# Kernel optimization log

Measured on AMD Instinct MI355X. Metric: run time of the kernel, lower is better.

Reference implementation:

```python
import math
import jax, jax.numpy as jnp
import numpy as np


def setup_inputs() -> dict:
    key = jax.random.key(0)
    k1, k2, k3 = jax.random.split(key, 3)
    mk = jax.random.normal(k1, (4, 64, 8, 32, 32), dtype=jnp.float32)
    qk = jax.random.normal(k2, (4, 64, 32, 32), dtype=jnp.float32)
    mv = jax.random.normal(k3, (4, 512, 8, 32, 32), dtype=jnp.float32)
    return {"mk": mk, "qk": qk, "mv": mv}


def reference(mk, qk, mv):
    B, CK, T, H, W = mk.shape
    CV = mv.shape[1]
    mkf = mk.reshape(B, CK, T * H * W)          # [B, CK, N]  (memory tokens)
    qkf = qk.reshape(B, CK, H * W)              # [B, CK, M]  (query tokens)
    # L2-distance style affinity: (2*a.b - |a|^2) / sqrt(CK)
    a_sq = jnp.sum(mkf * mkf, axis=1)[:, :, None]              # [B, N, 1]
    ab = jnp.einsum('bcn,bcm->bnm', mkf, qkf)                  # [B, N, M]
    affinity = (2.0 * ab - a_sq) / math.sqrt(CK)
    affinity = jax.nn.softmax(affinity, axis=1)                # softmax over memory dim
    # readout: weighted sum of memory values
    mo = mv.reshape(B, CV, T * H * W)                          # [B, CV, N]
    mem = jnp.einsum('bcn,bnm->bcm', mo, affinity)             # [B, CV, M]
    return mem.reshape(B, CV, H, W)
```

## Files before the change

kernel.cpp:

```cpp
#include <hip/hip_runtime.h>


typedef unsigned short ushort_t;
typedef unsigned int uint_t;
typedef __attribute__((ext_vector_type(8))) short short8;
typedef __attribute__((ext_vector_type(4))) float floatx4;

#define MFMA16(a, b, c) __builtin_amdgcn_mfma_f32_16x16x32_bf16((a), (b), (c), 0, 0, 0)

__device__ __forceinline__ ushort_t f2b(float f) {
    uint_t b = __float_as_uint(f);
    b += 0x7FFFu + ((b >> 16) & 1u);
    return (ushort_t)(b >> 16);
}

#define BB 4
#define CK 64
#define NN 8192
#define MM 1024
#define CV 512
#define NSTEP 128

__device__ __align__(16) ushort_t g_mkT[BB * NN * CK];
__device__ __align__(16) float    g_asq8[BB * NN];
__device__ __align__(16) ushort_t g_mvb[BB * CV * NN];

__global__ __launch_bounds__(256) void k_prep(const float* __restrict__ mk) {
    int t = blockIdx.x * 256 + threadIdx.x;
    int b = t >> 13;
    int n = t & (NN - 1);
    const float* src = mk + (size_t)b * CK * NN + n;
    ushort_t* dst = g_mkT + (size_t)t * CK;
    float acc = 0.f;
#pragma unroll
    for (int g = 0; g < 8; g++) {
        float f[8];
#pragma unroll
        for (int i = 0; i < 8; i++) {
            f[i] = src[(size_t)(g * 8 + i) * NN];
            acc += f[i] * f[i];
        }
        uint4 q;
        q.x = (uint_t)f2b(f[0]) | ((uint_t)f2b(f[1]) << 16);
        q.y = (uint_t)f2b(f[2]) | ((uint_t)f2b(f[3]) << 16);
        q.z = (uint_t)f2b(f[4]) | ((uint_t)f2b(f[5]) << 16);
        q.w = (uint_t)f2b(f[6]) | ((uint_t)f2b(f[7]) << 16);
        *(uint4*)(dst + g * 8) = q;
    }
    g_asq8[t] = acc * 0.125f;
}

__global__ __launch_bounds__(256) void k_mvconv(const float* __restrict__ mv) {
    size_t t = (size_t)blockIdx.x * 256 + threadIdx.x;
    const float4* s = (const float4*)mv + t * 2;
    float4 x = s[0], y = s[1];
    uint4 q;
    q.x = (uint_t)f2b(x.x) | ((uint_t)f2b(x.y) << 16);
    q.y = (uint_t)f2b(x.z) | ((uint_t)f2b(x.w) << 16);
    q.z = (uint_t)f2b(y.x) | ((uint_t)f2b(y.y) << 16);
    q.w = (uint_t)f2b(y.z) | ((uint_t)f2b(y.w) << 16);
    ((uint4*)g_mvb)[t] = q;
}

__global__ __launch_bounds__(256, 2) void k_main(const float* __restrict__ qk,
                                                 float* __restrict__ out) {
    __shared__ __align__(16) ushort_t ktile[2][64 * 64];
    __shared__ __align__(16) ushort_t lds_p[64 * 72];
    __shared__ __align__(16) float    asq_s[2][64];
    __shared__ float denom_s[64];

    int bx = blockIdx.x;
    int mt16 = bx >> 5;
    int cs = (bx >> 2) & 7;
    int b = bx & 3;
    int c0 = cs * 64;
    int m0 = mt16 * 64;

    int tid = threadIdx.x;
    int w = tid >> 6;
    int lane = tid & 63;
    int quad = lane >> 4;
    int l15 = lane & 15;

    int mrow = m0 + w * 16 + l15;
    short8 aq0, aq1;
#pragma unroll
    for (int j = 0; j < 8; j++) {
        aq0[j] = (short)f2b(qk[(size_t)(b * CK + quad * 8 + j) * MM + mrow]);
        aq1[j] = (short)f2b(qk[(size_t)(b * CK + 32 + quad * 8 + j) * MM + mrow]);
    }

    const ushort_t* mkTb = g_mkT + (size_t)b * NN * CK;

    floatx4 acc[4];
#pragma unroll
    for (int j = 0; j < 4; j++) acc[j] = (floatx4){0.f, 0.f, 0.f, 0.f};
    float dpart[4] = {0.f, 0.f, 0.f, 0.f};
    int mbase = w * 16 + quad * 4;

    {
#pragma unroll
        for (int gi = 0; gi < 2; gi++) {
            int g2 = w + gi * 4;
            const ushort_t* gsrc = mkTb + (size_t)lane * CK + g2 * 8;
            ushort_t* ldst = &ktile[0][g2 * 512];
            __builtin_amdgcn_global_load_lds(
                (const __attribute__((address_space(1))) unsigned int*)gsrc,
                (__attribute__((address_space(3))) unsigned int*)ldst, 16, 0, 0);
        }
        if (w == 0) {
            const float* as = g_asq8 + (size_t)b * NN + lane;
            __builtin_amdgcn_global_load_lds(
                (const __attribute__((address_space(1))) unsigned int*)as,
                (__attribute__((address_space(3))) unsigned int*)&asq_s[0][0], 4, 0, 0);
        }
    }
    __syncthreads();

    for (int step = 0; step < NSTEP; step++) {
        int buf = step & 1;
        int n0 = step * 64;

#pragma unroll
        for (int nt = 0; nt < 4; nt++) {
            int nl = nt * 16 + l15;
            const ushort_t* kr = &ktile[buf][(quad * 64 + nl) * 8];
            short8 kb0 = *(const short8*)kr;
            short8 kb1 = *(const short8*)(kr + 2048);
            floatx4 d = {0.f, 0.f, 0.f, 0.f};
            d = MFMA16(aq0, kb0, d);
            d = MFMA16(aq1, kb1, d);
            float sa = asq_s[buf][nl];
#pragma unroll
            for (int r = 0; r < 4; r++) {
                float p = __expf(d[r] * 0.25f - sa);
                dpart[r] += p;
                lds_p[(mbase + r) * 72 + nl] = f2b(p);
            }
        }
        __syncthreads();

        if (step + 1 < NSTEP) {
            int nb = buf ^ 1;
            int n1 = n0 + 64;
#pragma unroll
            for (int gi = 0; gi < 2; gi++) {
                int g2 = w + gi * 4;
                const ushort_t* gsrc = mkTb + (size_t)(n1 + lane) * CK + g2 * 8;
                ushort_t* ldst = &ktile[nb][g2 * 512];
                __builtin_amdgcn_global_load_lds(
                    (const __attribute__((address_space(1))) unsigned int*)gsrc,
                    (__attribute__((address_space(3))) unsigned int*)ldst, 16, 0, 0);
            }
            if (w == 0) {
                const float* as = g_asq8 + (size_t)b * NN + n1 + lane;
                __builtin_amdgcn_global_load_lds(
                    (const __attribute__((address_space(1))) unsigned int*)as,
                    (__attribute__((address_space(3))) unsigned int*)&asq_s[nb][0], 4, 0, 0);
            }
        }

#pragma unroll
        for (int kc = 0; kc < 2; kc++) {
            short8 pb[4];
#pragma unroll
            for (int mt = 0; mt < 4; mt++)
                pb[mt] = *(const short8*)&lds_p[(mt * 16 + l15) * 72 + kc * 32 + quad * 8];
            size_t vidx = (size_t)(b * CV + c0 + w * 16 + l15) * NN + n0 + kc * 32 + quad * 8;
            short8 va = *(const short8*)(g_mvb + vidx);
#pragma unroll
            for (int mt = 0; mt < 4; mt++)
                acc[mt] = MFMA16(va, pb[mt], acc[mt]);
        }
        __syncthreads();
    }

#pragma unroll
    for (int off = 1; off < 16; off <<= 1) {
#pragma unroll
        for (int r = 0; r < 4; r++) dpart[r] += __shfl_xor(dpart[r], off, 64);
    }
    if (l15 == 0) {
#pragma unroll
        for (int r = 0; r < 4; r++) denom_s[w * 16 + quad * 4 + r] = dpart[r];
    }
    __syncthreads();

#pragma unroll
    for (int mt = 0; mt < 4; mt++) {
        float rdm = 1.0f / denom_s[mt * 16 + l15];
#pragma unroll
        for (int r = 0; r < 4; r++) {
            size_t o = (size_t)(b * CV + c0 + w * 16 + quad * 4 + r) * MM + m0 + mt * 16 + l15;
            out[o] = acc[mt][r] * rdm;
        }
    }
}

extern "C" void kernel_launch(void* const* d_in, const int* in_sizes, int n_in,
                              void* d_out, int out_size, void* d_ws, size_t ws_size,
                              hipStream_t stream) {
    const float* mk = nullptr;
    const float* qk = nullptr;
    const float* mv = nullptr;
    for (int i = 0; i < n_in; i++) {
        if (in_sizes[i] == BB * CK * NN)      mk = (const float*)d_in[i];
        else if (in_sizes[i] == BB * CK * MM) qk = (const float*)d_in[i];
        else if (in_sizes[i] == BB * CV * NN) mv = (const float*)d_in[i];
    }
    float* out = (float*)d_out;
    (void)d_ws; (void)ws_size; (void)out_size;

    const size_t mv_elems = (size_t)BB * CV * NN;

    k_prep<<<(BB * NN) / 256, 256, 0, stream>>>(mk);
    k_mvconv<<<(int)(mv_elems / (8 * 256)), 256, 0, stream>>>(mv);
    k_main<<<16 * 8 * BB, 256, 0, stream>>>(qk, out);
}
```

Before: 292.4 us.

## Halve query tile per block, split memory columns across waves, double-buffer P

The main kernel now handles 32 query rows per block instead of 64, which doubles the grid. The four waves are split into 2 query halves × 2 memory-column halves for the affinity step, and partial softmax denominators are combined through shared memory. The P tile is double-buffered so one barrier per step can be removed, and the occupancy hint rises to 4 blocks per CU. The mk prep kernel is rewritten to transpose through shared memory for coalesced reads. The cost is that each block re-reads mv twice as often overall, since value reuse per block is halved, which raises global traffic on the dominant mv stream.

Result: slower. 336.0 us (+14.9%).

```diff
diff --git a/kernel.cpp b/kernel.cpp
--- a/kernel.cpp
+++ b/kernel.cpp
@@ -26,28 +26,46 @@
 __device__ __align__(16) ushort_t g_mvb[BB * CV * NN];
 
 __global__ __launch_bounds__(256) void k_prep(const float* __restrict__ mk) {
-    int t = blockIdx.x * 256 + threadIdx.x;
-    int b = t >> 13;
-    int n = t & (NN - 1);
-    const float* src = mk + (size_t)b * CK * NN + n;
-    ushort_t* dst = g_mkT + (size_t)t * CK;
-    float acc = 0.f;
-#pragma unroll
-    for (int g = 0; g < 8; g++) {
-        float f[8];
-#pragma unroll
-        for (int i = 0; i < 8; i++) {
-            f[i] = src[(size_t)(g * 8 + i) * NN];
-            acc += f[i] * f[i];
-        }
-        uint4 q;
-        q.x = (uint_t)f2b(f[0]) | ((uint_t)f2b(f[1]) << 16);
-        q.y = (uint_t)f2b(f[2]) | ((uint_t)f2b(f[3]) << 16);
-        q.z = (uint_t)f2b(f[4]) | ((uint_t)f2b(f[5]) << 16);
-        q.w = (uint_t)f2b(f[6]) | ((uint_t)f2b(f[7]) << 16);
-        *(uint4*)(dst + g * 8) = q;
-    }
-    g_asq8[t] = acc * 0.125f;
+    __shared__ float T[64][65];
+    int blk = blockIdx.x;
+    int b = blk >> 7;
+    int n0 = (blk & 127) * 64;
+    int tid = threadIdx.x;
+
+#pragma unroll
+    for (int it = 0; it < 16; it++) {
+        int c = it * 4 + (tid >> 6);
+        int n = tid & 63;
+        T[n][c] = mk[(size_t)(b * CK + c) * NN + n0 + n];
+    }
+    __syncthreads();
+
+    int n = tid >> 2;
+    int seg = tid & 3;
+    float s = 0.f;
+    ushort_t v[16];
+#pragma unroll
+    for (int i = 0; i < 16; i++) {
+        float f = T[n][seg * 16 + i];
+        s += f * f;
+        v[i] = f2b(f);
+    }
+    uint4 q0, q1;
+    q0.x = (uint_t)v[0] | ((uint_t)v[1] << 16);
+    q0.y = (uint_t)v[2] | ((uint_t)v[3] << 16);
+    q0.z = (uint_t)v[4] | ((uint_t)v[5] << 16);
+    q0.w = (uint_t)v[6] | ((uint_t)v[7] << 16);
+    q1.x = (uint_t)v[8] | ((uint_t)v[9] << 16);
+    q1.y = (uint_t)v[10] | ((uint_t)v[11] << 16);
+    q1.z = (uint_t)v[12] | ((uint_t)v[13] << 16);
+    q1.w = (uint_t)v[14] | ((uint_t)v[15] << 16);
+    ushort_t* dst = g_mkT + (size_t)(b * NN + n0 + n) * CK + seg * 16;
+    *(uint4*)dst = q0;
+    *(uint4*)(dst + 8) = q1;
+
+    s += __shfl_xor(s, 1, 64);
+    s += __shfl_xor(s, 2, 64);
+    if (seg == 0) g_asq8[b * NN + n0 + n] = s * 0.125f;
 }
 
 __global__ __launch_bounds__(256) void k_mvconv(const float* __restrict__ mv) {
@@ -62,27 +80,29 @@
     ((uint4*)g_mvb)[t] = q;
 }
 
-__global__ __launch_bounds__(256, 2) void k_main(const float* __restrict__ qk,
+__global__ __launch_bounds__(256, 4) void k_main(const float* __restrict__ qk,
                                                  float* __restrict__ out) {
     __shared__ __align__(16) ushort_t ktile[2][64 * 64];
-    __shared__ __align__(16) ushort_t lds_p[64 * 72];
+    __shared__ __align__(16) ushort_t lds_p[2][32 * 72];
     __shared__ __align__(16) float    asq_s[2][64];
-    __shared__ float denom_s[64];
+    __shared__ float denom_s[2][32];
 
     int bx = blockIdx.x;
-    int mt16 = bx >> 5;
+    int mt32 = bx >> 5;
     int cs = (bx >> 2) & 7;
     int b = bx & 3;
     int c0 = cs * 64;
-    int m0 = mt16 * 64;
+    int m0 = mt32 * 32;
 
     int tid = threadIdx.x;
     int w = tid >> 6;
     int lane = tid & 63;
     int quad = lane >> 4;
     int l15 = lane & 15;
-
-    int mrow = m0 + w * 16 + l15;
+    int mh = w >> 1;
+    int nh = w & 1;
+
+    int mrow = m0 + mh * 16 + l15;
     short8 aq0, aq1;
 #pragma unroll
     for (int j = 0; j < 8; j++) {
@@ -92,28 +112,23 @@
 
     const ushort_t* mkTb = g_mkT + (size_t)b * NN * CK;
 
-    floatx4 acc[4];
-#pragma unroll
-    for (int j = 0; j < 4; j++) acc[j] = (floatx4){0.f, 0.f, 0.f, 0.f};
+    floatx4 acc[2];
+    acc[0] = (floatx4){0.f, 0.f, 0.f, 0.f};
+    acc[1] = (floatx4){0.f, 0.f, 0.f, 0.f};
     float dpart[4] = {0.f, 0.f, 0.f, 0.f};
-    int mbase = w * 16 + quad * 4;
-
-    {
-#pragma unroll
-        for (int gi = 0; gi < 2; gi++) {
-            int g2 = w + gi * 4;
-            const ushort_t* gsrc = mkTb + (size_t)lane * CK + g2 * 8;
-            ushort_t* ldst = &ktile[0][g2 * 512];
-            __builtin_amdgcn_global_load_lds(
-                (const __attribute__((address_space(1))) unsigned int*)gsrc,
-                (__attribute__((address_space(3))) unsigned int*)ldst, 16, 0, 0);
-        }
-        if (w == 0) {
-            const float* as = g_asq8 + (size_t)b * NN + lane;
-            __builtin_amdgcn_global_load_lds(
-                (const __attribute__((address_space(1))) unsigned int*)as,
-                (__attribute__((address_space(3))) unsigned int*)&asq_s[0][0], 4, 0, 0);
-        }
+
+#pragma unroll
+    for (int gi = 0; gi < 2; gi++) {
+        int g2 = w + gi * 4;
+        const ushort_t* gsrc = mkTb + (size_t)lane * CK + g2 * 8;
+        __builtin_amdgcn_global_load_lds(
+            (const __attribute__((address_space(1))) unsigned int*)gsrc,
+            (__attribute__((address_space(3))) unsigned int*)&ktile[0][g2 * 512], 16, 0, 0);
+    }
+    if (w == 0) {
+        __builtin_amdgcn_global_load_lds(
+            (const __attribute__((address_space(1))) unsigned int*)(g_asq8 + (size_t)b * NN + lane),
+            (__attribute__((address_space(3))) unsigned int*)&asq_s[0][0], 4, 0, 0);
     }
     __syncthreads();
 
@@ -122,57 +137,51 @@
         int n0 = step * 64;
 
 #pragma unroll
-        for (int nt = 0; nt < 4; nt++) {
-            int nl = nt * 16 + l15;
-            const ushort_t* kr = &ktile[buf][(quad * 64 + nl) * 8];
+        for (int tt = 0; tt < 2; tt++) {
+            int col = nh * 32 + tt * 16 + l15;
+            const ushort_t* kr = &ktile[buf][(quad * 64 + col) * 8];
             short8 kb0 = *(const short8*)kr;
             short8 kb1 = *(const short8*)(kr + 2048);
             floatx4 d = {0.f, 0.f, 0.f, 0.f};
             d = MFMA16(aq0, kb0, d);
             d = MFMA16(aq1, kb1, d);
-            float sa = asq_s[buf][nl];
+            float sa = asq_s[buf][col];
 #pragma unroll
             for (int r = 0; r < 4; r++) {
                 float p = __expf(d[r] * 0.25f - sa);
                 dpart[r] += p;
-                lds_p[(mbase + r) * 72 + nl] = f2b(p);
+                lds_p[buf][(mh * 16 + quad * 4 + r) * 72 + col] = f2b(p);
             }
         }
-        __syncthreads();
 
         if (step + 1 < NSTEP) {
-            int nb = buf ^ 1;
             int n1 = n0 + 64;
 #pragma unroll
             for (int gi = 0; gi < 2; gi++) {
                 int g2 = w + gi * 4;
                 const ushort_t* gsrc = mkTb + (size_t)(n1 + lane) * CK + g2 * 8;
-                ushort_t* ldst = &ktile[nb][g2 * 512];
                 __builtin_amdgcn_global_load_lds(
                     (const __attribute__((address_space(1))) unsigned int*)gsrc,
-                    (__attribute__((address_space(3))) unsigned int*)ldst, 16, 0, 0);
+                    (__attribute__((address_space(3))) unsigned int*)&ktile[buf ^ 1][g2 * 512], 16, 0, 0);
             }
             if (w == 0) {
-                const float* as = g_asq8 + (size_t)b * NN + n1 + lane;
                 __builtin_amdgcn_global_load_lds(
-                    (const __attribute__((address_space(1))) unsigned int*)as,
-                    (__attribute__((address_space(3))) unsigned int*)&asq_s[nb][0], 4, 0, 0);
+                    (const __attribute__((address_space(1))) unsigned int*)(g_asq8 + (size_t)b * NN + n1 + lane),
+                    (__attribute__((address_space(3))) unsigned int*)&asq_s[buf ^ 1][0], 4, 0, 0);
             }
         }
 
+        __syncthreads();
+
 #pragma unroll
         for (int kc = 0; kc < 2; kc++) {
-            short8 pb[4];
-#pragma unroll
-            for (int mt = 0; mt < 4; mt++)
-                pb[mt] = *(const short8*)&lds_p[(mt * 16 + l15) * 72 + kc * 32 + quad * 8];
+            short8 pb0 = *(const short8*)&lds_p[buf][(0 * 16 + l15) * 72 + kc * 32 + quad * 8];
+            short8 pb1 = *(const short8*)&lds_p[buf][(1 * 16 + l15) * 72 + kc * 32 + quad * 8];
             size_t vidx = (size_t)(b * CV + c0 + w * 16 + l15) * NN + n0 + kc * 32 + quad * 8;
             short8 va = *(const short8*)(g_mvb + vidx);
-#pragma unroll
-            for (int mt = 0; mt < 4; mt++)
-                acc[mt] = MFMA16(va, pb[mt], acc[mt]);
-        }
-        __syncthreads();
+            acc[0] = MFMA16(va, pb0, acc[0]);
+            acc[1] = MFMA16(va, pb1, acc[1]);
+        }
     }
 
 #pragma unroll
@@ -182,16 +191,17 @@
     }
     if (l15 == 0) {
 #pragma unroll
-        for (int r = 0; r < 4; r++) denom_s[w * 16 + quad * 4 + r] = dpart[r];
+        for (int r = 0; r < 4; r++) denom_s[nh][mh * 16 + quad * 4 + r] = dpart[r];
     }
     __syncthreads();
 
 #pragma unroll
-    for (int mt = 0; mt < 4; mt++) {
-        float rdm = 1.0f / denom_s[mt * 16 + l15];
+    for (int mt = 0; mt < 2; mt++) {
+        int m = mt * 16 + l15;
+        float rdm = 1.0f / (denom_s[0][m] + denom_s[1][m]);
 #pragma unroll
         for (int r = 0; r < 4; r++) {
-            size_t o = (size_t)(b * CV + c0 + w * 16 + quad * 4 + r) * MM + m0 + mt * 16 + l15;
+            size_t o = (size_t)(b * CV + c0 + w * 16 + quad * 4 + r) * MM + m0 + m;
             out[o] = acc[mt][r] * rdm;
         }
     }
@@ -213,7 +223,7 @@
 
     const size_t mv_elems = (size_t)BB * CV * NN;
 
-    k_prep<<<(BB * NN) / 256, 256, 0, stream>>>(mk);
+    k_prep<<<(BB * NN) / 64, 256, 0, stream>>>(mk);
     k_mvconv<<<(int)(mv_elems / (8 * 256)), 256, 0, stream>>>(mv);
-    k_main<<<16 * 8 * BB, 256, 0, stream>>>(qk, out);
-}
+    k_main<<<32 * 8 * BB, 256, 0, stream>>>(qk, out);
+}
```
